# Kernel optimization log

Measured on AMD Instinct MI355X. Metric: run time of the kernel, lower is better.

## Reference

```python
import jax, jax.numpy as jnp
import numpy as np

B, S, D, H = 4, 2048, 1024, 16
DK = D // H

def setup_inputs() -> dict:
    key = jax.random.key(0)
    ks = jax.random.split(key, 5)
    scale = D ** -0.5  # keep activations well-scaled for random weights
    return {
        "x": jax.random.normal(ks[0], (B, S, D), dtype=jnp.float32),
        "w_q": jax.random.normal(ks[1], (D, D), dtype=jnp.float32) * scale,
        "w_k": jax.random.normal(ks[2], (D, D), dtype=jnp.float32) * scale,
        "w_v": jax.random.normal(ks[3], (D, D), dtype=jnp.float32) * scale,
        "w_o": jax.random.normal(ks[4], (D, D), dtype=jnp.float32) * scale,
        "b_o": jnp.zeros((D,), dtype=jnp.float32),
    }

def reference(x, w_q, w_k, w_v, w_o, b_o):
    b, s, d = x.shape
    # nn.Linear applies x @ W^T; project then split heads -> [b, h, s, dk]
    q = (x @ w_q.T).reshape(b, s, H, DK).transpose(0, 2, 1, 3)
    k = (x @ w_k.T).reshape(b, s, H, DK).transpose(0, 2, 1, 3)
    v = (x @ w_v.T).reshape(b, s, H, DK).transpose(0, 2, 1, 3)
    scores = jnp.einsum('bhqd,bhkd->bhqk', q, k) * (DK ** -0.5)
    causal = jnp.tril(jnp.ones((s, s), dtype=bool))  # [s, s]
    scores = jnp.where(causal, scores, jnp.float32(-1e9))
    attn = jax.nn.softmax(scores, axis=-1)
    out = jnp.einsum('bhqk,bhkd->bhqd', attn, v)
    out = out.transpose(0, 2, 1, 3).reshape(b, s, d)
    return out @ w_o.T + b_o
```

## Files before the change

### kernel.cpp

```cpp
#include <hip/hip_runtime.h>

typedef unsigned short u16;
typedef unsigned int u32;
typedef __attribute__((ext_vector_type(4))) u16 u16x4;
typedef __attribute__((ext_vector_type(8))) short short8;
typedef __attribute__((ext_vector_type(4))) float f32x4;
typedef __attribute__((ext_vector_type(16))) float f32x16;
typedef __attribute__((ext_vector_type(4))) u32 uint4v;

#define AS1 __attribute__((address_space(1)))
#define AS3 __attribute__((address_space(3)))

#define B_  4
#define S_  2048
#define D_  1024
#define H_  16
#define DK_ 64

#define WAIT_VM(n) asm volatile("s_waitcnt vmcnt(" #n ")" ::: "memory")
#define WAIT_LGK0  asm volatile("s_waitcnt lgkmcnt(0)" ::: "memory")

__device__ __forceinline__ u16 f2bf(float f) {
  union { float f; unsigned u; } v; v.f = f;
  unsigned r = v.u + 0x7fffu + ((v.u >> 16) & 1u);
  return (u16)(r >> 16);
}

__device__ __forceinline__ u32 cvt_pk_bf16(float lo, float hi) {
  u32 r;
  asm("v_cvt_pk_bf16_f32 %0, %1, %2" : "=v"(r) : "v"(lo), "v"(hi));
  return r;
}

__device__ __forceinline__ void pl32_swap(u32& a, u32& b) {
  asm("v_permlane32_swap_b32 %0, %1" : "+v"(a), "+v"(b));
}

__device__ __forceinline__ void gload_lds16(const void* g, void* l) {
  __builtin_amdgcn_global_load_lds((const AS1 void*)g, (AS3 void*)l, 16, 0, 0);
}

__global__ __launch_bounds__(256) void conv_bf16(const float* __restrict__ in,
                                                 u16* __restrict__ out,
                                                 int n, float scale) {
  int i = (blockIdx.x * 256 + threadIdx.x) * 8;
  if (i >= n) return;
  f32x4 a = *reinterpret_cast<const f32x4*>(in + i);
  f32x4 b = *reinterpret_cast<const f32x4*>(in + i + 4);
  union { u16 u[8]; uint4v v; } r;
#pragma unroll
  for (int j = 0; j < 4; ++j) {
    r.u[j]     = f2bf(a[j] * scale);
    r.u[4 + j] = f2bf(b[j] * scale);
  }
  *reinterpret_cast<uint4v*>(out + i) = r.v;
}

__global__ __launch_bounds__(256) void conv_w4(const float* __restrict__ w0,
                                               const float* __restrict__ w1,
                                               const float* __restrict__ w2,
                                               const float* __restrict__ w3,
                                               u16* __restrict__ out, float s0) {
  int y = blockIdx.y;
  const float* src = (y == 0) ? w0 : (y == 1) ? w1 : (y == 2) ? w2 : w3;
  float scale = (y == 0) ? s0 : 1.0f;
  int i = (blockIdx.x * 256 + threadIdx.x) * 8;
  f32x4 a = *reinterpret_cast<const f32x4*>(src + i);
  f32x4 b = *reinterpret_cast<const f32x4*>(src + i + 4);
  union { u16 u[8]; uint4v v; } r;
#pragma unroll
  for (int j = 0; j < 4; ++j) {
    r.u[j]     = f2bf(a[j] * scale);
    r.u[4 + j] = f2bf(b[j] * scale);
  }
  *reinterpret_cast<uint4v*>(out + (size_t)y * (D_ * D_) + i) = r.v;
}

template<int MODE>
__global__ __launch_bounds__(256) void gemm_bt(const u16* __restrict__ A,
                                               const u16* __restrict__ B,
                                               u16* __restrict__ Qb,
                                               u16* __restrict__ Kb,
                                               u16* __restrict__ Vt,
                                               float* __restrict__ Cf,
                                               const float* __restrict__ bias,
                                               int M, int N, int K) {
  __shared__ __attribute__((aligned(16))) u16 As[128 * 64];
  __shared__ __attribute__((aligned(16))) u16 Bs[128 * 64];

  const int t = threadIdx.x;
  const int l = t & 63;
  const int w = t >> 6;
  const int wr = w >> 1, wc = w & 1;
  const int m0 = blockIdx.y * 128;
  const int n0 = blockIdx.x * 128;

  f32x4 zero = {0.f, 0.f, 0.f, 0.f};
  f32x4 acc[4][4];
#pragma unroll
  for (int i = 0; i < 4; ++i)
#pragma unroll
    for (int j = 0; j < 4; ++j) acc[i][j] = zero;

  for (int k0 = 0; k0 < K; k0 += 64) {
    __syncthreads();
#pragma unroll
    for (int i = 0; i < 4; ++i) {
      int slot = i * 256 + t;
      int r = slot >> 3, c = slot & 7;
      const u16* srcA = A + (size_t)(m0 + r) * K + k0 + ((c ^ (r & 7)) * 8);
      gload_lds16(srcA, (char*)As + (size_t)(i * 256 + w * 64) * 16);
      const u16* srcB = B + (size_t)(n0 + r) * K + k0 + ((c ^ (r & 7)) * 8);
      gload_lds16(srcB, (char*)Bs + (size_t)(i * 256 + w * 64) * 16);
    }
    __syncthreads();

#pragma unroll
    for (int kc = 0; kc < 2; ++kc) {
      short8 a[4], bf[4];
      int lc = kc * 4 + (l >> 4);
#pragma unroll
      for (int i = 0; i < 4; ++i) {
        int ra = wr * 64 + i * 16 + (l & 15);
        a[i] = *reinterpret_cast<const short8*>(&As[ra * 64 + ((lc ^ (ra & 7)) * 8)]);
        int rb = wc * 64 + i * 16 + (l & 15);
        bf[i] = *reinterpret_cast<const short8*>(&Bs[rb * 64 + ((lc ^ (rb & 7)) * 8)]);
      }
#pragma unroll
      for (int mi = 0; mi < 4; ++mi)
#pragma unroll
        for (int ni = 0; ni < 4; ++ni)
          acc[mi][ni] = __builtin_amdgcn_mfma_f32_16x16x32_bf16(a[mi], bf[ni], acc[mi][ni], 0, 0, 0);
    }
  }

#pragma unroll
  for (int ni = 0; ni < 4; ++ni) {
    int col = n0 + wc * 64 + ni * 16 + (l & 15);
    float bv = (MODE == 1) ? bias[col] : 0.f;
#pragma unroll
    for (int mi = 0; mi < 4; ++mi) {
      int row0 = m0 + wr * 64 + mi * 16 + (l >> 4) * 4;
      if (MODE == 1) {
#pragma unroll
        for (int r = 0; r < 4; ++r)
          Cf[(size_t)(row0 + r) * N + col] = acc[mi][ni][r] + bv;
      } else {
        if (col < 2048) {
          u16* dst = (col < 1024) ? Qb : Kb;
          int c = col & 1023;
#pragma unroll
          for (int r = 0; r < 4; ++r)
            dst[(size_t)(row0 + r) * 1024 + c] = f2bf(acc[mi][ni][r]);
        } else {
          int vc = col - 2048;
          int bh = (row0 >> 11) * 16 + (vc >> 6);
          int s0 = row0 & 2047;
          u16x4 pk;
#pragma unroll
          for (int r = 0; r < 4; ++r) pk[r] = f2bf(acc[mi][ni][r]);
          *reinterpret_cast<u16x4*>(Vt + ((size_t)(bh * 64 + (vc & 63))) * 2048 + s0) = pk;
        }
      }
    }
  }
}

__global__ __launch_bounds__(256) void attn_fwd(const u16* __restrict__ Q,
                                                const u16* __restrict__ K,
                                                const u16* __restrict__ Vtg,
                                                u16* __restrict__ AO) {
  __shared__ __attribute__((aligned(16))) u16 smem[24576];
  u16* Ksb = smem;
  u16* Vsb = smem + 12288;

  const int t = threadIdx.x;
  const int l = t & 63;
  const int w = t >> 6;
  const int hi = l >> 5;
  const int hi8 = hi * 8, hi4 = hi * 4;
  const int bh = blockIdx.x;
  const int s = 15 - blockIdx.y;
  const size_t qkbase = (size_t)((bh >> 4) * S_) * D_ + (bh & 15) * DK_;
  const u16* Vg = Vtg + (size_t)bh * 64 * S_;

  const int qw = s * 128 + w * 32;
  const int qi = qw + (l & 31);

  short8 qf[4];
#pragma unroll
  for (int c = 0; c < 4; ++c)
    qf[c] = *reinterpret_cast<const short8*>(Q + qkbase + (size_t)qi * D_ + c * 16 + hi8);

  f32x16 o0 = {0,0,0,0,0,0,0,0,0,0,0,0,0,0,0,0};
  f32x16 o1 = {0,0,0,0,0,0,0,0,0,0,0,0,0,0,0,0};
  float l_r = 0.f;

  const int nst = 2 * (s + 1);

  auto stage = [&](int jt, u16* kdst, u16* vdst) {
    const u16* Ksrc = K + qkbase + (size_t)(jt * 64) * D_;
    const u16* Vsrc = Vg + jt * 64;
#pragma unroll
    for (int i = 0; i < 2; ++i) {
      int slot = i * 256 + t;
      int r = slot >> 3, c = t & 7;
      gload_lds16(Ksrc + (size_t)r * D_ + ((c ^ (r & 7)) * 8),
                  (char*)kdst + (size_t)(i * 256 + w * 64) * 16);
      gload_lds16(Vsrc + (size_t)r * S_ + ((c ^ (r & 7)) * 8),
                  (char*)vdst + (size_t)(i * 256 + w * 64) * 16);
    }
  };

  stage(0, Ksb, Vsb);
  stage(1, Ksb + 4096, Vsb + 4096);
  stage(2, Ksb + 8192, Vsb + 8192);
  int o0b = 0, o1b = 4096, o2b = 8192;

  for (int it = 0; it < nst; ++it) {
    if (it < nst - 2)       { WAIT_VM(8); }
    else if (it == nst - 2) { WAIT_VM(4); }
    else                    { WAIT_VM(0); }
    __builtin_amdgcn_s_barrier();
    __builtin_amdgcn_sched_barrier(0);

    const int j0 = it * 64;
    u16* ks = Ksb + o0b;
    u16* vs = Vsb + o0b;

    if (j0 <= qw + 31) {
      f32x16 s0 = {0,0,0,0,0,0,0,0,0,0,0,0,0,0,0,0};
      f32x16 s1 = {0,0,0,0,0,0,0,0,0,0,0,0,0,0,0,0};
#pragma unroll
      for (int c = 0; c < 4; ++c) {
        int cl = 2 * c + hi;
        int k0r = l & 31, k1r = (l & 31) + 32;
        short8 kf0 = *reinterpret_cast<const short8*>(&ks[k0r * 64 + ((cl ^ (k0r & 7)) * 8)]);
        short8 kf1 = *reinterpret_cast<const short8*>(&ks[k1r * 64 + ((cl ^ (k1r & 7)) * 8)]);
        s0 = __builtin_amdgcn_mfma_f32_32x32x16_bf16(kf0, qf[c], s0, 0, 0, 0);
        s1 = __builtin_amdgcn_mfma_f32_32x32x16_bf16(kf1, qf[c], s1, 0, 0, 0);
      }
      if (j0 + 63 > qw) {
#pragma unroll
        for (int r = 0; r < 16; ++r) {
          int key = j0 + (r & 3) + 8 * (r >> 2) + hi4;
          if (key > qi) s0[r] = -INFINITY;
          if (key + 32 > qi) s1[r] = -INFINITY;
        }
      }
      {
        float sum = 0.f;
#pragma unroll
        for (int r = 0; r < 16; ++r) { s0[r] = exp2f(s0[r]); sum += s0[r]; }
#pragma unroll
        for (int r = 0; r < 16; ++r) { s1[r] = exp2f(s1[r]); sum += s1[r]; }
        sum += __shfl_xor(sum, 32);
        l_r += sum;
      }
#pragma unroll
      for (int ksl = 0; ksl < 4; ++ksl) {
        const int b = 8 * (ksl & 1);
        const f32x16& ps = (ksl < 2) ? s0 : s1;
        u32 c0 = cvt_pk_bf16(ps[b + 0], ps[b + 1]);
        u32 c1 = cvt_pk_bf16(ps[b + 2], ps[b + 3]);
        u32 c2 = cvt_pk_bf16(ps[b + 4], ps[b + 5]);
        u32 c3 = cvt_pk_bf16(ps[b + 6], ps[b + 7]);
        pl32_swap(c0, c2);
        pl32_swap(c1, c3);
        union { u32 u[4]; short8 s; } pa;
        pa.u[0] = c0; pa.u[1] = c1; pa.u[2] = c2; pa.u[3] = c3;
        int cl = 2 * ksl + hi;
        int d0r = l & 31, d1r = (l & 31) + 32;
        short8 vf0 = *reinterpret_cast<const short8*>(&vs[d0r * 64 + ((cl ^ (d0r & 7)) * 8)]);
        short8 vf1 = *reinterpret_cast<const short8*>(&vs[d1r * 64 + ((cl ^ (d1r & 7)) * 8)]);
        o0 = __builtin_amdgcn_mfma_f32_32x32x16_bf16(vf0, pa.s, o0, 0, 0, 0);
        o1 = __builtin_amdgcn_mfma_f32_32x32x16_bf16(vf1, pa.s, o1, 0, 0, 0);
      }
    }

    WAIT_LGK0;
    __builtin_amdgcn_sched_barrier(0);
    __builtin_amdgcn_s_barrier();
    if (it + 3 < nst) stage(it + 3, Ksb + o0b, Vsb + o0b);
    int tmp = o0b; o0b = o1b; o1b = o2b; o2b = tmp;
  }

  float inv = 1.0f / l_r;
  u16* Ob = smem + w * 2304;
#pragma unroll
  for (int acc = 0; acc < 2; ++acc) {
    const f32x16& oo = acc ? o1 : o0;
#pragma unroll
    for (int rp = 0; rp < 8; ++rp) {
      u32 pk = cvt_pk_bf16(oo[2 * rp] * inv, oo[2 * rp + 1] * inv);
      int d0 = ((2 * rp) & 3) + 8 * (rp >> 1) + hi4 + 32 * acc;
      *reinterpret_cast<u32*>(&Ob[(l & 31) * 72 + d0]) = pk;
    }
  }
  __syncthreads();
  int qq = l >> 1;
  int chb = (l & 1) * 4;
#pragma unroll
  for (int c2 = 0; c2 < 4; ++c2) {
    uint4v vv = *reinterpret_cast<const uint4v*>(&Ob[qq * 72 + (chb + c2) * 8]);
    *reinterpret_cast<uint4v*>(&AO[qkbase + (size_t)(qw + qq) * D_ + (chb + c2) * 8]) = vv;
  }
}

extern "C" void kernel_launch(void* const* d_in, const int* in_sizes, int n_in,
                              void* d_out, int out_size, void* d_ws, size_t ws_size,
                              hipStream_t stream) {
  const float* x  = (const float*)d_in[0];
  const float* wq = (const float*)d_in[1];
  const float* wk = (const float*)d_in[2];
  const float* wv = (const float*)d_in[3];
  const float* wo = (const float*)d_in[4];
  const float* bo = (const float*)d_in[5];
  float* out = (float*)d_out;

  char* ws = (char*)d_ws;
  u16* XB   = (u16*)(ws);
  u16* WQKV = (u16*)(ws + (size_t)(16 << 20));
  u16* WOB  = (u16*)(ws + (size_t)(22 << 20));
  u16* Qb   = (u16*)(ws + (size_t)(24 << 20));
  u16* Kb   = (u16*)(ws + (size_t)(40 << 20));
  u16* Vt   = (u16*)(ws + (size_t)(56 << 20));
  u16* AO   = (u16*)(ws + (size_t)(72 << 20));

  const int nx = B_ * S_ * D_;
  const int nw = D_ * D_;

  conv_bf16<<<nx / 2048, 256, 0, stream>>>(x, XB, nx, 1.0f);
  conv_w4<<<dim3(nw / 2048, 4), 256, 0, stream>>>(wq, wk, wv, wo, WQKV,
                                                  0.18033688011112042f);

  gemm_bt<0><<<dim3(3072 / 128, (B_ * S_) / 128), 256, 0, stream>>>(
      XB, WQKV, Qb, Kb, Vt, nullptr, nullptr, B_ * S_, 3072, D_);

  attn_fwd<<<dim3(B_ * H_, 16), 256, 0, stream>>>(Qb, Kb, Vt, AO);

  gemm_bt<1><<<dim3(D_ / 128, (B_ * S_) / 128), 256, 0, stream>>>(
      AO, WOB, nullptr, nullptr, nullptr, out, bo, B_ * S_, D_, D_);
}
```

Measured before the change: 179.3 us.

## Remap GEMM blocks across XCDs and widen attention blocks to 8 waves

```diff
diff --git a/kernel.cpp b/kernel.cpp
--- a/kernel.cpp
+++ b/kernel.cpp
@@ -84,7 +84,7 @@
                                                u16* __restrict__ Vt,
                                                float* __restrict__ Cf,
                                                const float* __restrict__ bias,
-                                               int M, int N, int K) {
+                                               int M, int N, int K, int nbx) {
   __shared__ __attribute__((aligned(16))) u16 As[128 * 64];
   __shared__ __attribute__((aligned(16))) u16 Bs[128 * 64];
 
@@ -92,8 +92,11 @@
   const int l = t & 63;
   const int w = t >> 6;
   const int wr = w >> 1, wc = w & 1;
-  const int m0 = blockIdx.y * 128;
-  const int n0 = blockIdx.x * 128;
+  const int dd = blockIdx.x;
+  const int cpx = gridDim.x >> 3;
+  const int lid = (dd & 7) * cpx + (dd >> 3);
+  const int m0 = (lid / nbx) * 128;
+  const int n0 = (lid % nbx) * 128;
 
   f32x4 zero = {0.f, 0.f, 0.f, 0.f};
   f32x4 acc[4][4];
@@ -166,7 +169,7 @@
   }
 }
 
-__global__ __launch_bounds__(256) void attn_fwd(const u16* __restrict__ Q,
+__global__ __launch_bounds__(512) void attn_fwd(const u16* __restrict__ Q,
                                                 const u16* __restrict__ K,
                                                 const u16* __restrict__ Vtg,
                                                 u16* __restrict__ AO) {
@@ -180,11 +183,12 @@
   const int hi = l >> 5;
   const int hi8 = hi * 8, hi4 = hi * 4;
   const int bh = blockIdx.x;
-  const int s = 15 - blockIdx.y;
+  const int by = blockIdx.y;
+  const int s = (by < 4) ? (7 - 2 * by) : (2 * (by - 4));
   const size_t qkbase = (size_t)((bh >> 4) * S_) * D_ + (bh & 15) * DK_;
   const u16* Vg = Vtg + (size_t)bh * 64 * S_;
 
-  const int qw = s * 128 + w * 32;
+  const int qw = s * 256 + w * 32;
   const int qi = qw + (l & 31);
 
   short8 qf[4];
@@ -196,20 +200,16 @@
   f32x16 o1 = {0,0,0,0,0,0,0,0,0,0,0,0,0,0,0,0};
   float l_r = 0.f;
 
-  const int nst = 2 * (s + 1);
+  const int nst = 4 * (s + 1);
 
   auto stage = [&](int jt, u16* kdst, u16* vdst) {
     const u16* Ksrc = K + qkbase + (size_t)(jt * 64) * D_;
     const u16* Vsrc = Vg + jt * 64;
-#pragma unroll
-    for (int i = 0; i < 2; ++i) {
-      int slot = i * 256 + t;
-      int r = slot >> 3, c = t & 7;
-      gload_lds16(Ksrc + (size_t)r * D_ + ((c ^ (r & 7)) * 8),
-                  (char*)kdst + (size_t)(i * 256 + w * 64) * 16);
-      gload_lds16(Vsrc + (size_t)r * S_ + ((c ^ (r & 7)) * 8),
-                  (char*)vdst + (size_t)(i * 256 + w * 64) * 16);
-    }
+    int r = t >> 3, c = t & 7;
+    gload_lds16(Ksrc + (size_t)r * D_ + ((c ^ (r & 7)) * 8),
+                (char*)kdst + (size_t)t * 16);
+    gload_lds16(Vsrc + (size_t)r * S_ + ((c ^ (r & 7)) * 8),
+                (char*)vdst + (size_t)t * 16);
   };
 
   stage(0, Ksb, Vsb);
@@ -218,8 +218,8 @@
   int o0b = 0, o1b = 4096, o2b = 8192;
 
   for (int it = 0; it < nst; ++it) {
-    if (it < nst - 2)       { WAIT_VM(8); }
-    else if (it == nst - 2) { WAIT_VM(4); }
+    if (it < nst - 2)       { WAIT_VM(4); }
+    else if (it == nst - 2) { WAIT_VM(2); }
     else                    { WAIT_VM(0); }
     __builtin_amdgcn_s_barrier();
     __builtin_amdgcn_sched_barrier(0);
@@ -334,11 +334,11 @@
   conv_w4<<<dim3(nw / 2048, 4), 256, 0, stream>>>(wq, wk, wv, wo, WQKV,
                                                   0.18033688011112042f);
 
-  gemm_bt<0><<<dim3(3072 / 128, (B_ * S_) / 128), 256, 0, stream>>>(
-      XB, WQKV, Qb, Kb, Vt, nullptr, nullptr, B_ * S_, 3072, D_);
-
-  attn_fwd<<<dim3(B_ * H_, 16), 256, 0, stream>>>(Qb, Kb, Vt, AO);
-
-  gemm_bt<1><<<dim3(D_ / 128, (B_ * S_) / 128), 256, 0, stream>>>(
-      AO, WOB, nullptr, nullptr, nullptr, out, bo, B_ * S_, D_, D_);
-}
+  gemm_bt<0><<<1536, 256, 0, stream>>>(
+      XB, WQKV, Qb, Kb, Vt, nullptr, nullptr, B_ * S_, 3072, D_, 24);
+
+  attn_fwd<<<dim3(B_ * H_, 8), 512, 0, stream>>>(Qb, Kb, Vt, AO);
+
+  gemm_bt<1><<<512, 256, 0, stream>>>(
+      AO, WOB, nullptr, nullptr, nullptr, out, bo, B_ * S_, D_, D_, 8);
+}
```

Result: faster. 171.3 us (-4.4%).
